# Optimization experiments

Hardware: AMD Instinct MI355X
Metric: run time of the kernel (lower is better)

## Reference

```python
import jax, jax.numpy as jnp
import numpy as np

N_NODES = 50000
N_EDGES = 1600000
D_IN = 64
D_OUT = 64
N_REL = 32


def setup_inputs() -> dict:
    key = jax.random.key(0)
    k_h, k_w, k_src, k_dst, k_rel, k_norm = jax.random.split(key, 6)
    h = jax.random.normal(k_h, (N_NODES, D_IN), dtype=jnp.float32)
    W = jax.random.normal(k_w, (N_REL, D_IN, D_OUT), dtype=jnp.float32) * 0.05
    src = jax.random.randint(k_src, (N_EDGES,), 0, N_NODES, dtype=jnp.int32)
    dst = jax.random.randint(k_dst, (N_EDGES,), 0, N_NODES, dtype=jnp.int32)
    rel_type = jax.random.randint(k_rel, (N_EDGES,), 0, N_REL, dtype=jnp.int32)
    norm = jax.random.uniform(k_norm, (N_EDGES,), dtype=jnp.float32)
    return {"h": h, "W": W, "src": src, "dst": dst, "rel_type": rel_type, "norm": norm}


def reference(h, W, src, dst, rel_type, norm):
    # R-GCN message passing (is_input=False branch):
    #   msg_e = (W[rel_type_e] applied to h[src_e]) * norm_e
    #   h'_v  = sum_{e: dst_e = v} msg_e
    # Instead of gathering a [E, D_IN, D_OUT] weight tensor per edge (26 GB),
    # precompute h @ W for all (node, relation) pairs -- mathematically
    # identical since W[r] h[n] = (hW)[n, r] -- then gather per edge.
    n_nodes = h.shape[0]
    per_node_rel = jnp.einsum('ni,rio->nro', h, W)            # [N, R, D_OUT]
    msg = per_node_rel[src, rel_type] * norm[:, None]         # [E, D_OUT]
    out = jax.ops.segment_sum(msg, dst, num_segments=n_nodes)  # [N, D_OUT]
    return out
```

## Files before the change

kernel.cpp:

```cpp
#include <hip/hip_runtime.h>


#define N_NODES 50000
#define N_EDGES 1600000
#define D 64
#define N_REL 32

#define BSHIFT 7
#define NPB 128
#define NB 391
#define EPB 4096
#define SC_BLOCKS 391
#define SORT_CAP 6144
#define NKEY 256

typedef __attribute__((ext_vector_type(8))) __bf16 bf16x8;
typedef __attribute__((ext_vector_type(4))) __bf16 bf16x4;
typedef __attribute__((ext_vector_type(4))) float f32x4;
typedef __attribute__((ext_vector_type(4))) _Float16 f16x4;

static __device__ inline unsigned short f16_bits(_Float16 v) {
    union { _Float16 f; unsigned short u; } cv; cv.f = v; return cv.u;
}
static __device__ inline _Float16 bits_f16(unsigned short u) {
    union { _Float16 f; unsigned short u; } cv; cv.u = u; return cv.f;
}


__global__ __launch_bounds__(512) void k_zeroc(int* __restrict__ gcnt) {
    if (threadIdx.x < NB) gcnt[threadIdx.x] = 0;
}

__global__ __launch_bounds__(256) void k_hist2(const int* __restrict__ dst,
                                               int* __restrict__ gcnt) {
    __shared__ int lc[NB];
    for (int b = threadIdx.x; b < NB; b += 256) lc[b] = 0;
    __syncthreads();
    const int e0 = blockIdx.x * EPB;
    #pragma unroll
    for (int j = 0; j < 16; ++j) {
        int e = e0 + j * 256 + threadIdx.x;
        if (e < N_EDGES) atomicAdd(&lc[dst[e] >> BSHIFT], 1);
    }
    __syncthreads();
    for (int b = threadIdx.x; b < NB; b += 256)
        if (lc[b]) atomicAdd(&gcnt[b], lc[b]);
}

__global__ __launch_bounds__(512) void k_scanc(const int* __restrict__ gcnt,
                                               int* __restrict__ base,
                                               int* __restrict__ cur) {
    const int t = threadIdx.x;
    const int lane = t & 63;
    const int w = t >> 6;
    int v = (t < NB) ? gcnt[t] : 0;
    int x = v;
    #pragma unroll
    for (int d = 1; d < 64; d <<= 1) {
        int n = __shfl_up(x, d, 64);
        if (lane >= d) x += n;
    }
    __shared__ int wt[8];
    if (lane == 63) wt[w] = x;
    __syncthreads();
    if (t == 0) {
        int run = 0;
        #pragma unroll
        for (int i = 0; i < 8; ++i) { int tmp = wt[i]; wt[i] = run; run += tmp; }
    }
    __syncthreads();
    int excl = x - v + wt[w];
    if (t < NB) { base[t] = excl; cur[t] = excl; }
    if (t == NB - 1) base[NB] = excl + v;
}

__global__ __launch_bounds__(256) void k_scatter2(
        const int* __restrict__ src, const int* __restrict__ dst,
        const int* __restrict__ rel, const float* __restrict__ norm,
        int* __restrict__ cur, int2* __restrict__ pay) {
    __shared__ int cnt[NB];
    __shared__ int bl[NB + 1];
    __shared__ int gb[NB];
    __shared__ unsigned short bid[EPB];
    __shared__ int2 stage[EPB];
    __shared__ int wt[8];

    const int t = threadIdx.x;
    const int lane = t & 63;
    const int w = t >> 6;
    const int e0 = blockIdx.x * EPB;

    for (int b = t; b < NB; b += 256) cnt[b] = 0;
    __syncthreads();

    #pragma unroll
    for (int j = 0; j < 16; ++j) {
        int e = e0 + j * 256 + t;
        if (e < N_EDGES) atomicAdd(&cnt[dst[e] >> BSHIFT], 1);
    }
    __syncthreads();

    {
        int x0 = (t < NB) ? cnt[t] : 0;
        int x1 = (t + 256 < NB) ? cnt[t + 256] : 0;
        int s0 = x0, s1 = x1;
        #pragma unroll
        for (int d = 1; d < 64; d <<= 1) {
            int n0 = __shfl_up(s0, d, 64);
            int n1 = __shfl_up(s1, d, 64);
            if (lane >= d) { s0 += n0; s1 += n1; }
        }
        if (lane == 63) { wt[w] = s0; wt[4 + w] = s1; }
        __syncthreads();
        if (t == 0) {
            int run = 0;
            #pragma unroll
            for (int i = 0; i < 8; ++i) { int tmp = wt[i]; wt[i] = run; run += tmp; }
        }
        __syncthreads();
        int ex0 = s0 - x0 + wt[w];
        int ex1 = s1 - x1 + wt[4 + w];
        if (t < NB) bl[t] = ex0;
        if (t + 256 < NB) bl[t + 256] = ex1;
        if (t == 0) {
            int tot = (e0 + EPB <= N_EDGES) ? EPB : (N_EDGES > e0 ? N_EDGES - e0 : 0);
            bl[NB] = tot;
        }
    }
    __syncthreads();

    for (int b = t; b < NB; b += 256) {
        int c = bl[b + 1] - bl[b];
        gb[b] = c ? atomicAdd(&cur[b], c) : 0;
    }
    for (int b = t; b < NB; b += 256) cnt[b] = 0;
    __syncthreads();

    #pragma unroll
    for (int j = 0; j < 16; ++j) {
        int e = e0 + j * 256 + t;
        if (e < N_EDGES) {
            int dv = dst[e];
            int b = dv >> BSHIFT;
            int r = atomicAdd(&cnt[b], 1);
            int pos = bl[b] + r;
            stage[pos] = make_int2(((dv & (NPB - 1)) << 21) | (rel[e] << 16) | src[e],
                                   __float_as_int(norm[e]));
            bid[pos] = (unsigned short)b;
        }
    }
    __syncthreads();

    const int total = bl[NB];
    for (int p = t; p < total; p += 256) {
        int b = bid[p];
        pay[gb[b] + (p - bl[b])] = stage[p];
    }
}

__global__ __launch_bounds__(512) void k_sort(
        const int* __restrict__ base, int2* __restrict__ pay,
        int* __restrict__ runs) {
    __shared__ int2 stage[SORT_CAP];
    __shared__ int cnt[8][NKEY];
    __shared__ int wb[8][NKEY];
    __shared__ int kbase[NKEY];
    __shared__ int wsum[8];

    const int t = threadIdx.x;
    const int lane = t & 63;
    const int w = t >> 6;
    const int b = blockIdx.x;
    const int s = base[b];
    const int e = base[b + 1];
    const int n = min(e - s, SORT_CAP);

    for (int j = t; j < 8 * NKEY; j += 512) ((int*)cnt)[j] = 0;
    __syncthreads();

    for (int j = t; j < n; j += 512) {
        int2 p = pay[s + j];
        stage[j] = p;
        int key = (((p.x >> 25) & 7) << 5) | ((p.x >> 16) & 31);
        atomicAdd(&cnt[w][key], 1);
    }
    __syncthreads();

    int tot = 0;
    if (t < NKEY) {
        #pragma unroll
        for (int ww = 0; ww < 8; ++ww) tot += cnt[ww][t];
    }
    int x = tot;
    #pragma unroll
    for (int d = 1; d < 64; d <<= 1) {
        int nn = __shfl_up(x, d, 64);
        if (lane >= d) x += nn;
    }
    if (lane == 63) wsum[w] = x;
    __syncthreads();
    if (t == 0) {
        int run = 0;
        #pragma unroll
        for (int i = 0; i < 8; ++i) { int tmp = wsum[i]; wsum[i] = run; run += tmp; }
    }
    __syncthreads();
    int excl = x - tot + wsum[w];
    if (t < NKEY) kbase[t] = excl;
    __syncthreads();

    if (t < NKEY) {
        int run = kbase[t];
        #pragma unroll
        for (int ww = 0; ww < 8; ++ww) { wb[ww][t] = run; run += cnt[ww][t]; }
        runs[b * (NKEY + 1) + t] = s + kbase[t];
    }
    if (t == 0) runs[b * (NKEY + 1) + NKEY] = s + n;
    __syncthreads();
    for (int j = t; j < 8 * NKEY; j += 512) ((int*)cnt)[j] = 0;
    __syncthreads();

    for (int j = t; j < n; j += 512) {
        int2 p = stage[j];
        int key = (((p.x >> 25) & 7) << 5) | ((p.x >> 16) & 31);
        int pos = wb[w][key] + atomicAdd(&cnt[w][key], 1);
        pay[s + pos] = p;
    }
}

__global__ __launch_bounds__(256) void k_wconv(const float* __restrict__ W,
                                               __bf16* __restrict__ Wfrag) {
    const int r = blockIdx.x;
    const int lane = threadIdx.x & 63;
    const int jj = (threadIdx.x >> 6) * 2;
    const int q = lane >> 4;
    const int m = lane & 15;
    const float* Wr = W + (size_t)r * D * D;
    #pragma unroll
    for (int kt = 0; kt < 2; ++kt) {
        #pragma unroll
        for (int ot = 0; ot < 4; ++ot) {
            size_t dbase = ((((size_t)r * 2 + kt) * 4 + ot) * 64 + lane) * 8 + jj;
            Wfrag[dbase]     = (__bf16)Wr[(kt * 32 + q * 8 + jj) * D + ot * 16 + m];
            Wfrag[dbase + 1] = (__bf16)Wr[(kt * 32 + q * 8 + jj + 1) * D + ot * 16 + m];
        }
    }
}

__global__ __launch_bounds__(512) void k_hconv(const float* __restrict__ h,
                                               __bf16* __restrict__ hbf) {
    int idx = blockIdx.x * 512 + threadIdx.x;
    if (idx < N_NODES * 16) {
        float4 v = ((const float4*)h)[idx];
        bf16x4 o;
        o[0] = (__bf16)v.x; o[1] = (__bf16)v.y; o[2] = (__bf16)v.z; o[3] = (__bf16)v.w;
        ((bf16x4*)hbf)[idx] = o;
    }
}

__global__ __launch_bounds__(512) void k_fuse(
        const unsigned short* __restrict__ hbf, const __bf16* __restrict__ Wfrag,
        const int* __restrict__ runs, const int2* __restrict__ pay,
        float* __restrict__ out) {
    __shared__ int runsL[NKEY + 1];
    __shared__ __align__(16) unsigned short wbuf[2][4096];

    const int t = threadIdx.x;
    const int lane = t & 63;
    const int w = t >> 6;
    const int m = lane & 15;
    const int q = lane >> 4;
    const int b = blockIdx.x;

    for (int j = t; j < NKEY + 1; j += 512) runsL[j] = runs[b * (NKEY + 1) + j];
    ((bf16x8*)wbuf[0])[t] = ((const bf16x8*)Wfrag)[t];
    __syncthreads();

    const f32x4 vzero = {0.f, 0.f, 0.f, 0.f};
    f32x4 acc2[4];
    #pragma unroll
    for (int ot = 0; ot < 4; ++ot) acc2[ot] = vzero;

    for (int r = 0; r < N_REL; ++r) {
        bf16x8 nxt;
        if (r + 1 < N_REL) nxt = ((const bf16x8*)Wfrag)[(r + 1) * 512 + t];

        const int rs = runsL[w * 32 + r];
        const int re = runsL[w * 32 + r + 1];
        const unsigned short* wbp = wbuf[r & 1];

        if (re > rs) {
            bf16x8 wf[2][4];
            #pragma unroll
            for (int kt = 0; kt < 2; ++kt)
                #pragma unroll
                for (int ot = 0; ot < 4; ++ot)
                    wf[kt][ot] = *(const bf16x8*)(wbp + ((kt * 4 + ot) * 64 + lane) * 8);

            const int ntile = (re - rs + 15) >> 4;
            for (int tl = 0; tl < ntile; ++tl) {
                int ei = rs + tl * 16 + m;
                int2 p = pay[min(ei, re - 1)];
                float nvf = (ei < re) ? __int_as_float(p.y) : 0.f;
                int meta = (((p.x >> 21) & 15) << 16) | f16_bits((_Float16)nvf);

                const unsigned short* hrow = hbf + ((size_t)(p.x & 0xFFFF) << 6);
                bf16x8 a0 = *(const bf16x8*)(hrow + q * 8);
                bf16x8 a1 = *(const bf16x8*)(hrow + 32 + q * 8);

                f32x4 c1[4];
                #pragma unroll
                for (int ot = 0; ot < 4; ++ot) {
                    c1[ot] = __builtin_amdgcn_mfma_f32_16x16x32_bf16(a0, wf[0][ot], vzero, 0, 0, 0);
                    c1[ot] = __builtin_amdgcn_mfma_f32_16x16x32_bf16(a1, wf[1][ot], c1[ot], 0, 0, 0);
                }

                f16x4 a2;
                #pragma unroll
                for (int j = 0; j < 4; ++j) {
                    int sm = __shfl(meta, q * 4 + j, 64);
                    _Float16 nv = bits_f16((unsigned short)(sm & 0xFFFF));
                    a2[j] = ((sm >> 16) == m) ? nv : (_Float16)0.f;
                }

                #pragma unroll
                for (int ot = 0; ot < 4; ++ot) {
                    f16x4 b2;
                    b2[0] = (_Float16)c1[ot][0];
                    b2[1] = (_Float16)c1[ot][1];
                    b2[2] = (_Float16)c1[ot][2];
                    b2[3] = (_Float16)c1[ot][3];
                    acc2[ot] = __builtin_amdgcn_mfma_f32_16x16x16f16(a2, b2, acc2[ot], 0, 0, 0);
                }
            }
        }

        if (r + 1 < N_REL) ((bf16x8*)wbuf[(r + 1) & 1])[t] = nxt;
        __syncthreads();
    }

    const int node_base = b * NPB + w * 16;
    #pragma unroll
    for (int reg = 0; reg < 4; ++reg) {
        int node = node_base + q * 4 + reg;
        if (node < N_NODES) {
            float* orow = out + (size_t)node * D + m;
            #pragma unroll
            for (int ot = 0; ot < 4; ++ot)
                orow[ot * 16] = acc2[ot][reg];
        }
    }
}

extern "C" void kernel_launch(void* const* d_in, const int* in_sizes, int n_in,
                              void* d_out, int out_size, void* d_ws, size_t ws_size,
                              hipStream_t stream) {
    const float* h    = (const float*)d_in[0];
    const float* W    = (const float*)d_in[1];
    const int*   src  = (const int*)d_in[2];
    const int*   dst  = (const int*)d_in[3];
    const int*   rel  = (const int*)d_in[4];
    const float* norm = (const float*)d_in[5];
    float* out = (float*)d_out;

    char* ws = (char*)d_ws;
    int*    gcnt  = (int*)(ws);
    int*    base  = (int*)(ws + 0x1000);
    int*    cur   = (int*)(ws + 0x2000);
    int*    runs  = (int*)(ws + 0x3000);
    int2*   pay   = (int2*)(ws + 0x100000);
    __bf16* Wfrag = (__bf16*)(ws + 0xD40000);
    __bf16* hbf   = (__bf16*)(ws + 0xD80000);

    k_zeroc<<<1, 512, 0, stream>>>(gcnt);
    k_wconv<<<N_REL, 256, 0, stream>>>(W, Wfrag);
    k_hconv<<<1563, 512, 0, stream>>>(h, hbf);
    k_hist2<<<SC_BLOCKS, 256, 0, stream>>>(dst, gcnt);
    k_scanc<<<1, 512, 0, stream>>>(gcnt, base, cur);
    k_scatter2<<<SC_BLOCKS, 256, 0, stream>>>(src, dst, rel, norm, cur, pay);
    k_sort<<<NB, 512, 0, stream>>>(base, pay, runs);
    k_fuse<<<NB, 512, 0, stream>>>((const unsigned short*)hbf, Wfrag, runs, pay, out);
}
```

Before: 224.8 us.

## Software-pipeline edge payload and h-row gathers across tiles and relations

```diff
diff --git a/kernel.cpp b/kernel.cpp
--- a/kernel.cpp
+++ b/kernel.cpp
@@ -281,15 +281,48 @@
     #pragma unroll
     for (int ot = 0; ot < 4; ++ot) acc2[ot] = vzero;
 
+    const int kb = w * 32;
+
+    int pr = 0, ptl = 0, prs = 0, pre_ = 0;
+    while (pr < N_REL) { prs = runsL[kb + pr]; pre_ = runsL[kb + pr + 1]; if (pre_ > prs) break; ++pr; }
+
+    int cr = N_REL, cmask = 0;
+    int2 p_cur; bf16x8 a0c, a1c;
+    int nrel = N_REL, nmask = 0;
+    int2 p_nxt;
+
+    if (pr < N_REL) {
+        int ei = prs + ptl * 16 + m;
+        p_cur = pay[min(ei, pre_ - 1)];
+        cmask = (ei < pre_);
+        cr = pr;
+        ++ptl;
+        if (prs + ptl * 16 >= pre_) {
+            ++pr; ptl = 0;
+            while (pr < N_REL) { prs = runsL[kb + pr]; pre_ = runsL[kb + pr + 1]; if (pre_ > prs) break; ++pr; }
+        }
+        const unsigned short* hrow = hbf + ((size_t)(p_cur.x & 0xFFFF) << 6);
+        a0c = *(const bf16x8*)(hrow + q * 8);
+        a1c = *(const bf16x8*)(hrow + 32 + q * 8);
+        if (pr < N_REL) {
+            int ei2 = prs + ptl * 16 + m;
+            p_nxt = pay[min(ei2, pre_ - 1)];
+            nmask = (ei2 < pre_);
+            nrel = pr;
+            ++ptl;
+            if (prs + ptl * 16 >= pre_) {
+                ++pr; ptl = 0;
+                while (pr < N_REL) { prs = runsL[kb + pr]; pre_ = runsL[kb + pr + 1]; if (pre_ > prs) break; ++pr; }
+            }
+        }
+    }
+
     for (int r = 0; r < N_REL; ++r) {
-        bf16x8 nxt;
-        if (r + 1 < N_REL) nxt = ((const bf16x8*)Wfrag)[(r + 1) * 512 + t];
-
-        const int rs = runsL[w * 32 + r];
-        const int re = runsL[w * 32 + r + 1];
-        const unsigned short* wbp = wbuf[r & 1];
-
-        if (re > rs) {
+        bf16x8 stg;
+        if (r + 1 < N_REL) stg = ((const bf16x8*)Wfrag)[(r + 1) * 512 + t];
+
+        if (cr == r) {
+            const unsigned short* wbp = wbuf[r & 1];
             bf16x8 wf[2][4];
             #pragma unroll
             for (int kt = 0; kt < 2; ++kt)
@@ -297,22 +330,37 @@
                 for (int ot = 0; ot < 4; ++ot)
                     wf[kt][ot] = *(const bf16x8*)(wbp + ((kt * 4 + ot) * 64 + lane) * 8);
 
-            const int ntile = (re - rs + 15) >> 4;
-            for (int tl = 0; tl < ntile; ++tl) {
-                int ei = rs + tl * 16 + m;
-                int2 p = pay[min(ei, re - 1)];
-                float nvf = (ei < re) ? __int_as_float(p.y) : 0.f;
-                int meta = (((p.x >> 21) & 15) << 16) | f16_bits((_Float16)nvf);
-
-                const unsigned short* hrow = hbf + ((size_t)(p.x & 0xFFFF) << 6);
-                bf16x8 a0 = *(const bf16x8*)(hrow + q * 8);
-                bf16x8 a1 = *(const bf16x8*)(hrow + 32 + q * 8);
+            while (cr == r) {
+                int2 p_b = p_nxt;
+                int brel = nrel, bmask = nmask;
+                bf16x8 a0n, a1n;
+                if (brel < N_REL) {
+                    const unsigned short* hrn = hbf + ((size_t)(p_b.x & 0xFFFF) << 6);
+                    a0n = *(const bf16x8*)(hrn + q * 8);
+                    a1n = *(const bf16x8*)(hrn + 32 + q * 8);
+                }
+                if (pr < N_REL) {
+                    int ei2 = prs + ptl * 16 + m;
+                    p_nxt = pay[min(ei2, pre_ - 1)];
+                    nmask = (ei2 < pre_);
+                    nrel = pr;
+                    ++ptl;
+                    if (prs + ptl * 16 >= pre_) {
+                        ++pr; ptl = 0;
+                        while (pr < N_REL) { prs = runsL[kb + pr]; pre_ = runsL[kb + pr + 1]; if (pre_ > prs) break; ++pr; }
+                    }
+                } else {
+                    nrel = N_REL;
+                }
+
+                float nvf = cmask ? __int_as_float(p_cur.y) : 0.f;
+                int meta = (((p_cur.x >> 21) & 15) << 16) | f16_bits((_Float16)nvf);
 
                 f32x4 c1[4];
                 #pragma unroll
                 for (int ot = 0; ot < 4; ++ot) {
-                    c1[ot] = __builtin_amdgcn_mfma_f32_16x16x32_bf16(a0, wf[0][ot], vzero, 0, 0, 0);
-                    c1[ot] = __builtin_amdgcn_mfma_f32_16x16x32_bf16(a1, wf[1][ot], c1[ot], 0, 0, 0);
+                    c1[ot] = __builtin_amdgcn_mfma_f32_16x16x32_bf16(a0c, wf[0][ot], vzero, 0, 0, 0);
+                    c1[ot] = __builtin_amdgcn_mfma_f32_16x16x32_bf16(a1c, wf[1][ot], c1[ot], 0, 0, 0);
                 }
 
                 f16x4 a2;
@@ -332,10 +380,13 @@
                     b2[3] = (_Float16)c1[ot][3];
                     acc2[ot] = __builtin_amdgcn_mfma_f32_16x16x16f16(a2, b2, acc2[ot], 0, 0, 0);
                 }
+
+                p_cur = p_b; cmask = bmask; cr = brel;
+                a0c = a0n; a1c = a1n;
             }
         }
 
-        if (r + 1 < N_REL) ((bf16x8*)wbuf[(r + 1) & 1])[t] = nxt;
+        if (r + 1 < N_REL) ((bf16x8*)wbuf[(r + 1) & 1])[t] = stg;
         __syncthreads();
     }
 
```

After: 215.8 us. -4.0%, faster.
